# Performance work log

Hardware: AMD Instinct MI355X
Metric: run time of the kernel (lower is better)

Reference implementation:

```python
import jax, jax.numpy as jnp
import numpy as np

W_BIT = 4
HALF = 2 ** (W_BIT - 1)  # 8: recentering offset used in post_init
GROUP_SIZE = 128
IN_FEATURES = 4096
OUT_FEATURES = 11008
TOKENS = 32


def setup_inputs() -> dict:
    key = jax.random.key(0)
    k1, k2, k3, k4, k5 = jax.random.split(key, 5)
    n_groups = IN_FEATURES // GROUP_SIZE
    x = jax.random.normal(k1, (TOKENS, IN_FEATURES), dtype=jnp.float32)
    # unpacked 4-bit weight codes in [0, 15]
    qweight = jax.random.randint(k2, (IN_FEATURES, OUT_FEATURES), 0, 2 ** W_BIT, dtype=jnp.int32)
    # group-wise 4-bit zero-point codes in [0, 15]
    qzeros = jax.random.randint(k3, (n_groups, OUT_FEATURES), 0, 2 ** W_BIT, dtype=jnp.int32)
    # group-wise scales (positive, small, like real quant scales)
    scales = jax.random.uniform(k4, (n_groups, OUT_FEATURES), dtype=jnp.float32, minval=0.001, maxval=0.02)
    bias = jax.random.normal(k5, (OUT_FEATURES,), dtype=jnp.float32)
    return {"x": x, "qweight": qweight, "qzeros": qzeros, "scales": scales, "bias": bias}


def reference(x, qweight, qzeros, scales, bias):
    # post_init recenters codes: q -> q - 2^(b-1), z -> z - 2^(b-1)
    w_int = (qweight - HALF).astype(jnp.float32)            # [K, N]
    z_int = (qzeros - HALF).astype(jnp.float32)             # [K//gs, N]
    # broadcast group-wise zeros/scales along K
    z_rep = jnp.repeat(z_int, GROUP_SIZE, axis=0)           # [K, N]
    s_rep = jnp.repeat(scales, GROUP_SIZE, axis=0)          # [K, N]
    # fused dequant-GEMM: y = x @ ((q - z) * s) + bias
    w_deq = (w_int - z_rep) * s_rep                         # [K, N] fp32
    out = x @ w_deq + bias                                  # [T, N]
    return out
```

## Files before the change

kernel.cpp:

```cpp
#include <hip/hip_runtime.h>
#include <hip/hip_bf16.h>


#define TOKENS   32
#define KDIM     4096
#define NDIM     11008
#define GS       128
#define KSPLIT   8
#define KCHUNK   512
#define BLOCK    128
#define BLOCK_N  128

typedef __attribute__((ext_vector_type(8))) _Float16 half8;
typedef __attribute__((ext_vector_type(4))) float   floatx4;

__global__ __launch_bounds__(256) void awq_cvt_kernel(
    const float* __restrict__ x, unsigned short* __restrict__ xh)
{
    const int i = blockIdx.x * 256 + threadIdx.x;
    const float4 v = ((const float4*)x)[i];
    ushort4 o;
    o.x = __builtin_bit_cast(unsigned short, (_Float16)v.x);
    o.y = __builtin_bit_cast(unsigned short, (_Float16)v.y);
    o.z = __builtin_bit_cast(unsigned short, (_Float16)v.z);
    o.w = __builtin_bit_cast(unsigned short, (_Float16)v.w);
    ((ushort4*)xh)[i] = o;
}

__global__ __launch_bounds__(256) void awq_init_kernel(
    const float* __restrict__ bias, float* __restrict__ out)
{
    const int n = blockIdx.x * 256 + threadIdx.x;
    out[blockIdx.y * NDIM + n] = bias[n];
}

template<bool ATOMIC>
__global__ __launch_bounds__(BLOCK) void awq_gemm_mfma(
    const unsigned short* __restrict__ xh,
    const int*   __restrict__ qw,
    const int*   __restrict__ qz,
    const float* __restrict__ sc,
    float*       __restrict__ dst)
{
    const int tid  = threadIdx.x;
    const int lane = tid & 63;
    const int wv   = tid >> 6;
    const int col  = lane & 15;
    const int quad = lane >> 4;
    const int nb   = blockIdx.x * BLOCK_N + wv * 64;
    const int nc   = nb + 4 * col;

    floatx4 acc[4][2];
    #pragma unroll
    for (int nt = 0; nt < 4; ++nt) {
        acc[nt][0] = (floatx4){0.f, 0.f, 0.f, 0.f};
        acc[nt][1] = (floatx4){0.f, 0.f, 0.f, 0.f};
    }

    for (int gi = 0; gi < KCHUNK / GS; ++gi) {
        const int g   = blockIdx.y * (KCHUNK / GS) + gi;
        const int kc0 = g * GS;

        float s[4], nzs[4];
        #pragma unroll
        for (int nt = 0; nt < 4; ++nt) {
            const int n  = nc + nt;
            const float sv = sc[(size_t)g * NDIM + n];
            const int   zv = qz[(size_t)g * NDIM + n];
            s[nt] = sv; nzs[nt] = -(float)zv * sv;
        }

        const int* qbase = qw + (size_t)(kc0 + quad * 8) * NDIM + nc;
        const unsigned short* xr0 = xh + (size_t)col * KDIM + kc0 + quad * 8;
        const unsigned short* xr1 = xr0 + 16 * KDIM;

        #pragma unroll 2
        for (int ks = 0; ks < GS / 32; ++ks) {
            int4 q[8];
            #pragma unroll
            for (int j = 0; j < 8; ++j)
                q[j] = *(const int4*)(qbase + (size_t)(ks * 32 + j) * NDIM);

            const half8 a0 = *(const half8*)(xr0 + ks * 32);
            const half8 a1 = *(const half8*)(xr1 + ks * 32);

            half8 b0, b1, b2, b3;
            #pragma unroll
            for (int j = 0; j < 8; ++j) {
                b0[j] = (_Float16)fmaf((float)q[j].x, s[0], nzs[0]);
                b1[j] = (_Float16)fmaf((float)q[j].y, s[1], nzs[1]);
                b2[j] = (_Float16)fmaf((float)q[j].z, s[2], nzs[2]);
                b3[j] = (_Float16)fmaf((float)q[j].w, s[3], nzs[3]);
            }
            acc[0][0] = __builtin_amdgcn_mfma_f32_16x16x32_f16(a0, b0, acc[0][0], 0, 0, 0);
            acc[0][1] = __builtin_amdgcn_mfma_f32_16x16x32_f16(a1, b0, acc[0][1], 0, 0, 0);
            acc[1][0] = __builtin_amdgcn_mfma_f32_16x16x32_f16(a0, b1, acc[1][0], 0, 0, 0);
            acc[1][1] = __builtin_amdgcn_mfma_f32_16x16x32_f16(a1, b1, acc[1][1], 0, 0, 0);
            acc[2][0] = __builtin_amdgcn_mfma_f32_16x16x32_f16(a0, b2, acc[2][0], 0, 0, 0);
            acc[2][1] = __builtin_amdgcn_mfma_f32_16x16x32_f16(a1, b2, acc[2][1], 0, 0, 0);
            acc[3][0] = __builtin_amdgcn_mfma_f32_16x16x32_f16(a0, b3, acc[3][0], 0, 0, 0);
            acc[3][1] = __builtin_amdgcn_mfma_f32_16x16x32_f16(a1, b3, acc[3][1], 0, 0, 0);
        }
    }

    if (ATOMIC) {
        #pragma unroll
        for (int h = 0; h < 2; ++h)
            #pragma unroll
            for (int r = 0; r < 4; ++r) {
                float* pp = dst + (size_t)(h * 16 + quad * 4 + r) * NDIM + nc;
                unsafeAtomicAdd(pp + 0, acc[0][h][r]);
                unsafeAtomicAdd(pp + 1, acc[1][h][r]);
                unsafeAtomicAdd(pp + 2, acc[2][h][r]);
                unsafeAtomicAdd(pp + 3, acc[3][h][r]);
            }
    } else {
        float* pbase = dst + (size_t)blockIdx.y * TOKENS * NDIM;
        #pragma unroll
        for (int h = 0; h < 2; ++h)
            #pragma unroll
            for (int r = 0; r < 4; ++r) {
                const float4 v = make_float4(acc[0][h][r], acc[1][h][r],
                                             acc[2][h][r], acc[3][h][r]);
                *(float4*)(pbase + (size_t)(h * 16 + quad * 4 + r) * NDIM + nc) = v;
            }
    }
}

__global__ __launch_bounds__(256) void awq_reduce_kernel(
    const float* __restrict__ part,
    const float* __restrict__ bias,
    float*       __restrict__ out)
{
    const int o = blockIdx.x * 256 + threadIdx.x;
    const int t = o / (NDIM / 4);
    const int c = o - t * (NDIM / 4);
    const float4* p4 = (const float4*)part;
    float4 sum = ((const float4*)bias)[c];
    #pragma unroll
    for (int s = 0; s < KSPLIT; ++s) {
        const float4 v = p4[(size_t)(s * TOKENS + t) * (NDIM / 4) + c];
        sum.x += v.x; sum.y += v.y; sum.z += v.z; sum.w += v.w;
    }
    ((float4*)out)[o] = sum;
}

extern "C" void kernel_launch(void* const* d_in, const int* in_sizes, int n_in,
                              void* d_out, int out_size, void* d_ws, size_t ws_size,
                              hipStream_t stream) {
    const float* x    = (const float*)d_in[0];
    const int*   qw   = (const int*)  d_in[1];
    const int*   qz   = (const int*)  d_in[2];
    const float* sc   = (const float*)d_in[3];
    const float* bias = (const float*)d_in[4];
    float* out = (float*)d_out;

    const size_t xh_bytes   = 512 * 1024;
    const size_t part_bytes = (size_t)KSPLIT * TOKENS * NDIM * sizeof(float);
    unsigned short* xh = (unsigned short*)d_ws;
    float* part = (float*)((char*)d_ws + xh_bytes);

    awq_cvt_kernel<<<(TOKENS * KDIM / 4) / 256, 256, 0, stream>>>(x, xh);

    if (ws_size >= xh_bytes + part_bytes) {
        awq_gemm_mfma<false><<<dim3(NDIM / BLOCK_N, KSPLIT), BLOCK, 0, stream>>>(
            xh, qw, qz, sc, part);
        awq_reduce_kernel<<<(TOKENS * NDIM / 4) / 256, 256, 0, stream>>>(
            part, bias, out);
    } else {
        awq_init_kernel<<<dim3(NDIM / 256, TOKENS), 256, 0, stream>>>(bias, out);
        awq_gemm_mfma<true><<<dim3(NDIM / BLOCK_N, KSPLIT), BLOCK, 0, stream>>>(
            xh, qw, qz, sc, out);
    }
}
```

Before: 265.5 us.

## Split K across wave pairs within block and reduce partials via LDS

Doubles the block to 256 threads, with two waves per N-slice. Each wave in a pair handles half of the block's K chunk (two of the four groups), and the partial accumulators are summed through shared memory with a swizzled layout before the store. The aim is more waves in flight per block, to hide the latency of the weight loads. The cost is an LDS round trip, a barrier, and half the waves sitting idle during the epilogue.

```diff
diff --git a/kernel.cpp b/kernel.cpp
--- a/kernel.cpp
+++ b/kernel.cpp
@@ -8,7 +8,7 @@
 #define GS       128
 #define KSPLIT   8
 #define KCHUNK   512
-#define BLOCK    128
+#define BLOCK    256
 #define BLOCK_N  128
 
 typedef __attribute__((ext_vector_type(8))) _Float16 half8;
@@ -45,10 +45,14 @@
     const int tid  = threadIdx.x;
     const int lane = tid & 63;
     const int wv   = tid >> 6;
+    const int wv_n = wv & 1;
+    const int wv_k = wv >> 1;
     const int col  = lane & 15;
     const int quad = lane >> 4;
-    const int nb   = blockIdx.x * BLOCK_N + wv * 64;
+    const int nb   = blockIdx.x * BLOCK_N + wv_n * 64;
     const int nc   = nb + 4 * col;
+
+    __shared__ float4 red[2 * 64 * 8];
 
     floatx4 acc[4][2];
     #pragma unroll
@@ -57,8 +61,8 @@
         acc[nt][1] = (floatx4){0.f, 0.f, 0.f, 0.f};
     }
 
-    for (int gi = 0; gi < KCHUNK / GS; ++gi) {
-        const int g   = blockIdx.y * (KCHUNK / GS) + gi;
+    for (int gi = 0; gi < KCHUNK / GS / 2; ++gi) {
+        const int g   = blockIdx.y * (KCHUNK / GS) + wv_k * (KCHUNK / GS / 2) + gi;
         const int kc0 = g * GS;
 
         float s[4], nzs[4];
@@ -103,6 +107,32 @@
         }
     }
 
+    if (wv_k == 1) {
+        float4* rp = red + (size_t)(wv_n * 64 + lane) * 8;
+        #pragma unroll
+        for (int nt = 0; nt < 4; ++nt)
+            #pragma unroll
+            for (int h = 0; h < 2; ++h) {
+                const int js = ((nt * 2 + h) + (lane & 7)) & 7;
+                rp[js] = make_float4(acc[nt][h][0], acc[nt][h][1],
+                                     acc[nt][h][2], acc[nt][h][3]);
+            }
+    }
+    __syncthreads();
+    if (wv_k != 0) return;
+    {
+        const float4* rp = red + (size_t)(wv_n * 64 + lane) * 8;
+        #pragma unroll
+        for (int nt = 0; nt < 4; ++nt)
+            #pragma unroll
+            for (int h = 0; h < 2; ++h) {
+                const int js = ((nt * 2 + h) + (lane & 7)) & 7;
+                const float4 v = rp[js];
+                acc[nt][h][0] += v.x; acc[nt][h][1] += v.y;
+                acc[nt][h][2] += v.z; acc[nt][h][3] += v.w;
+            }
+    }
+
     if (ATOMIC) {
         #pragma unroll
         for (int h = 0; h < 2; ++h)
```

Measured after the change: 266.4 us. No clear change (+0.3%).
